# Performance work log

Hardware: AMD Instinct MI355X
Metric: run time of the kernel (lower is better)

Reference implementation:

```python
import jax, jax.numpy as jnp
import numpy as np

N = 10000      # atoms
E = 160000     # edges (avg degree 16)
H = 64         # hidden_channels
R = 64         # num_rbf
MAXZ = 100
RC = 4.5       # cutoff_upper (cutoff_lower = 0)
LN_EPS = 1e-5


def setup_inputs() -> dict:
    key = jax.random.key(0)
    ks = jax.random.split(key, 20)
    z = jax.random.randint(ks[0], (N,), 0, MAXZ, dtype=jnp.int32)
    edge_index = jax.random.randint(ks[1], (2, E), 0, N, dtype=jnp.int32)
    edge_weight = jax.random.uniform(ks[2], (E,), dtype=jnp.float32) * RC
    v = jax.random.normal(ks[3], (E, 3), dtype=jnp.float32)
    edge_vec_norm = v / jnp.linalg.norm(v, axis=-1, keepdims=True)
    edge_attr = jax.random.normal(ks[4], (E, R), dtype=jnp.float32)
    p = lambda k, shape: (jax.random.normal(k, shape, dtype=jnp.float32) * 0.1)
    return {
        'z': z, 'edge_index': edge_index, 'edge_weight': edge_weight,
        'edge_vec_norm': edge_vec_norm, 'edge_attr': edge_attr,
        'emb': p(ks[5], (MAXZ, H)),
        'emb2_w': p(ks[6], (H, 2 * H)), 'emb2_b': p(ks[7], (H,)),
        'dp1_w': p(ks[8], (H, R)), 'dp1_b': p(ks[9], (H,)),
        'dp2_w': p(ks[10], (H, R)), 'dp2_b': p(ks[11], (H,)),
        'dp3_w': p(ks[12], (H, R)), 'dp3_b': p(ks[13], (H,)),
        'ln_g': jnp.ones((H,), jnp.float32), 'ln_b': jnp.zeros((H,), jnp.float32),
        'w1': p(ks[14], (2 * H, H)), 'b1': jnp.zeros((2 * H,), jnp.float32),
        'w2': p(ks[15], (3 * H, 2 * H)), 'b2': jnp.zeros((3 * H,), jnp.float32),
        'm0': p(ks[16], (H, H)), 'm1': p(ks[17], (H, H)), 'm2': p(ks[18], (H, H)),
    }


def reference(z, edge_index, edge_weight, edge_vec_norm, edge_attr,
              emb, emb2_w, emb2_b, dp1_w, dp1_b, dp2_w, dp2_b, dp3_w, dp3_b,
              ln_g, ln_b, w1, b1, w2, b2, m0, m1, m2):
    n_atoms = z.shape[0]
    hc = emb.shape[1]
    src, dst = edge_index[0], edge_index[1]

    # atomic number message Z_ij: concat(Z_i, Z_j) -> Linear  [E,H]
    Zn = emb[z]
    Zij = jnp.concatenate([Zn[src], Zn[dst]], axis=-1) @ emb2_w.T + emb2_b

    # cosine cutoff (cutoff_lower == 0)
    C = 0.5 * (jnp.cos(edge_weight * jnp.pi / RC) + 1.0) * (edge_weight < RC)

    # RBF-gated per-edge channel weights, all [E,H]
    g1 = (edge_attr @ dp1_w.T + dp1_b) * C[:, None] * Zij
    g2 = (edge_attr @ dp2_w.T + dp2_b) * C[:, None] * Zij
    g3 = (edge_attr @ dp3_w.T + dp3_b) * C[:, None] * Zij

    eye = jnp.eye(3, dtype=Zij.dtype)
    vx, vy, vz = edge_vec_norm[:, 0], edge_vec_norm[:, 1], edge_vec_norm[:, 2]
    zero = jnp.zeros_like(vx)
    skew = jnp.stack([zero, -vz, vy, vz, zero, -vx, -vy, vx, zero], axis=-1).reshape(-1, 3, 3)
    outer = edge_vec_norm[:, :, None] * edge_vec_norm[:, None, :]  # [E,3,3], symmetric
    sym = outer - (jnp.trace(outer, axis1=-2, axis2=-1) / 3.0)[:, None, None] * eye

    # per-edge messages [E,H,3,3]
    Iij = g1[:, :, None, None] * eye
    Aij = g2[:, :, None, None] * skew[:, None, :, :]
    Sij = g3[:, :, None, None] * sym[:, None, :, :]

    # scatter-add to atoms
    I = jax.ops.segment_sum(Iij, src, num_segments=n_atoms)
    A = jax.ops.segment_sum(Aij, src, num_segments=n_atoms)
    S = jax.ops.segment_sum(Sij, src, num_segments=n_atoms)

    # tensor norm -> layernorm -> MLP1
    tn = ((I + A + S) ** 2).sum((-2, -1))  # [N,H]
    mu = tn.mean(-1, keepdims=True)
    var = ((tn - mu) ** 2).mean(-1, keepdims=True)
    norm = (tn - mu) / jnp.sqrt(var + LN_EPS) * ln_g + ln_b
    norm = jax.nn.silu(norm @ w1.T + b1)
    norm = jax.nn.silu(norm @ w2.T + b2)
    norm = norm.reshape(-1, hc, 3)
    n0 = norm[..., 0][:, :, None, None]

    # channel-mixing; NOTE: original code applies MLP2[1]/MLP2[2] to the
    # updated I and gates all three with norm[...,0] -- replicated faithfully.
    I = jnp.einsum('nhij,kh->nkij', I, m0) * n0
    A = jnp.einsum('nhij,kh->nkij', I, m1) * n0
    S = jnp.einsum('nhij,kh->nkij', I, m2) * n0
    return I + A + S
```

## Files before the change

kernel.cpp:

```cpp
#include <hip/hip_runtime.h>
#include <stdint.h>

#define NATOMS 10000
#define NEDGES 160000
#define RCUT   4.5f
#define CAP    64
#define ATGRID 2500
#define FGRID  1024

#define T_BYTES    ((size_t)NATOMS * 640 * 4)
#define CNT_OFF    (T_BYTES)
#define CNT_BYTES  ((size_t)NATOMS * 4)
#define REC_OFF    (CNT_OFF + CNT_BYTES)
#define REC_BYTES  ((size_t)NATOMS * CAP * 16)
#define EMB_OFF    (REC_OFF + REC_BYTES)
#define EMB_BYTES  ((size_t)100 * 64 * 2)
#define POS_OFF    (EMB_OFF + 0x4000)
#define POS_BYTES  ((size_t)NEDGES * 4)
#define ATTR2_OFF  (POS_OFF + 0xA0000)
#define ATTR2_BYTES ((size_t)NATOMS * CAP * 64 * 2)
#define WS_NEED    (ATTR2_OFF + ATTR2_BYTES)

typedef unsigned short u16;
typedef __bf16 bf16x8 __attribute__((ext_vector_type(8)));
typedef float  f32x4  __attribute__((ext_vector_type(4)));

#define MFMA16(a,b,c) __builtin_amdgcn_mfma_f32_16x16x32_bf16((a),(b),(c),0,0,0)
#define BFMAGIC 0x3F803F80u
#define MSK 0xffff0000u

__device__ __forceinline__ float uf(unsigned int u){ return __uint_as_float(u); }
__device__ __forceinline__ float b2f(u16 u){
  union { unsigned int i; float f; } v; v.i = ((unsigned int)u) << 16; return v.f;
}
__device__ __forceinline__ u16 f2b(float f){
  union { unsigned int i; float f; } v; v.f = f;
  unsigned int b = v.i + 0x7fffu + ((v.i >> 16) & 1u);
  return (u16)(b >> 16);
}
__device__ __forceinline__ float ldf(const void* p, int i, int bf){
  if (bf) return b2f(((const u16*)p)[i]);
  return ((const float*)p)[i];
}
__device__ __forceinline__ bf16x8 ld8bf(const void* p, int i, int bf){
  if (bf) return *(const bf16x8*)((const u16*)p + i);
  const float4* q = (const float4*)((const float*)p + i);
  float4 a = q[0], b = q[1];
  bf16x8 r;
  r[0]=(__bf16)a.x; r[1]=(__bf16)a.y; r[2]=(__bf16)a.z; r[3]=(__bf16)a.w;
  r[4]=(__bf16)b.x; r[5]=(__bf16)b.y; r[6]=(__bf16)b.z; r[7]=(__bf16)b.w;
  return r;
}
__device__ __forceinline__ uint4 ld8pk(const void* p, int i, int bf){
  if (bf) return *(const uint4*)((const u16*)p + i);
  const float4* q = (const float4*)((const float*)p + i);
  float4 a = q[0], b = q[1];
  uint4 r;
  r.x = (unsigned int)f2b(a.x) | ((unsigned int)f2b(a.y) << 16);
  r.y = (unsigned int)f2b(a.z) | ((unsigned int)f2b(a.w) << 16);
  r.z = (unsigned int)f2b(b.x) | ((unsigned int)f2b(b.y) << 16);
  r.w = (unsigned int)f2b(b.z) | ((unsigned int)f2b(b.w) << 16);
  return r;
}
__device__ __forceinline__ void ld8f(const void* p, int i, float* o, int bf){
  if (bf){
    uint4 v = *(const uint4*)((const u16*)p + i);
    o[0]=uf(v.x<<16); o[1]=uf(v.x&MSK); o[2]=uf(v.y<<16); o[3]=uf(v.y&MSK);
    o[4]=uf(v.z<<16); o[5]=uf(v.z&MSK); o[6]=uf(v.w<<16); o[7]=uf(v.w&MSK);
    return;
  }
  const float4* q = (const float4*)((const float*)p + i);
  float4 a = q[0], b = q[1];
  o[0]=a.x; o[1]=a.y; o[2]=a.z; o[3]=a.w; o[4]=b.x; o[5]=b.y; o[6]=b.z; o[7]=b.w;
}
__device__ __forceinline__ uint4 pk8(const float* f){
  uint4 r;
  r.x = (unsigned int)f2b(f[0]) | ((unsigned int)f2b(f[1]) << 16);
  r.y = (unsigned int)f2b(f[2]) | ((unsigned int)f2b(f[3]) << 16);
  r.z = (unsigned int)f2b(f[4]) | ((unsigned int)f2b(f[5]) << 16);
  r.w = (unsigned int)f2b(f[6]) | ((unsigned int)f2b(f[7]) << 16);
  return r;
}

__global__ __launch_bounds__(256) void scatter_kernel(const int* __restrict__ ei,
                                                      const int* __restrict__ z,
                                                      const void* __restrict__ ew,
                                                      const void* __restrict__ evn,
                                                      const void* __restrict__ emb,
                                                      u16* __restrict__ emb16,
                                                      int* __restrict__ cnt,
                                                      uint4* __restrict__ REC,
                                                      int* __restrict__ pos,
                                                      const unsigned int* __restrict__ lng){
  const int bf = (lng[0] == BFMAGIC);
  int e = blockIdx.x * 256 + threadIdx.x;
  if (e < 6400) emb16[e] = bf ? ((const u16*)emb)[e] : f2b(((const float*)emb)[e]);
  int s = ei[e], d = ei[NEDGES + e];
  int p = atomicAdd(&cnt[s], 1);
  const float w  = ldf(ew, e, bf);
  const float Cv = (w < RCUT) ? 0.5f*(__cosf(w * (3.14159265358979f / RCUT)) + 1.0f) : 0.0f;
  uint4 rec;
  rec.x = (unsigned int)e;
  rec.y = (unsigned int)z[d];
  rec.z = (unsigned int)f2b(ldf(evn, 3*e + 0, bf)) | ((unsigned int)f2b(ldf(evn, 3*e + 1, bf)) << 16);
  rec.w = (unsigned int)f2b(ldf(evn, 3*e + 2, bf)) | ((unsigned int)f2b(Cv) << 16);
  const int ok = (p < CAP);
  if (ok) REC[(size_t)s*CAP + p] = rec;
  if (pos) pos[e] = ok ? (s*CAP + p) : -1;
}

__global__ __launch_bounds__(256) void copy_kernel(const void* __restrict__ attr,
                                                   const int* __restrict__ pos,
                                                   u16* __restrict__ attr2,
                                                   const unsigned int* __restrict__ lng){
  const int bf  = (lng[0] == BFMAGIC);
  const int idx = blockIdx.x * 256 + threadIdx.x;
  const int e   = idx >> 3;
  const int c   = idx & 7;
  const int d   = pos[e];
  if (d >= 0)
    *(uint4*)(attr2 + (size_t)d*64 + c*8) = ld8pk(attr, e*64 + c*8, bf);
}

__global__ __launch_bounds__(256)
void atomT_stream(
    const int* __restrict__ z,
    const u16* __restrict__ emb16,
    const u16* __restrict__ attr2,
    const uint4* __restrict__ REC,
    const int* __restrict__ cnt,
    const void* __restrict__ e2w, const void* __restrict__ e2b,
    const void* __restrict__ d1w, const void* __restrict__ d1b,
    const void* __restrict__ d2w, const void* __restrict__ d2b,
    const void* __restrict__ d3w, const void* __restrict__ d3b,
    float* __restrict__ T,
    const unsigned int* __restrict__ lng)
{
  const int bf  = (lng[0] == BFMAGIC);
  const int tid = threadIdx.x;
  const int lane = tid & 63;
  const int wave = tid >> 6;
  const int hh   = lane & 15;
  const int quad = lane >> 4;
  const int h    = hh + 16*wave;

  const bf16x8 bw1a = ld8bf(d1w, h*64 + quad*8, bf);
  const bf16x8 bw1b = ld8bf(d1w, h*64 + 32 + quad*8, bf);
  const bf16x8 bw2a = ld8bf(d2w, h*64 + quad*8, bf);
  const bf16x8 bw2b = ld8bf(d2w, h*64 + 32 + quad*8, bf);
  const bf16x8 bw3a = ld8bf(d3w, h*64 + quad*8, bf);
  const bf16x8 bw3b = ld8bf(d3w, h*64 + 32 + quad*8, bf);
  const bf16x8 bea  = ld8bf(e2w, h*128 + quad*8, bf);
  const bf16x8 beb  = ld8bf(e2w, h*128 + 32 + quad*8, bf);
  const bf16x8 bec  = ld8bf(e2w, h*128 + 64 + quad*8, bf);
  const bf16x8 bed  = ld8bf(e2w, h*128 + 96 + quad*8, bf);

  const float be2 = ldf(e2b, h, bf);
  const float bd1 = ldf(d1b, h, bf);
  const float bd2 = ldf(d2b, h, bf);
  const float bd3 = ldf(d3b, h, bf);

  int n   = blockIdx.x;
  int cn  = cnt[n];
  int zsv = z[n];

  while (true) {
    const int e0   = n * CAP;
    const int nv   = min(cn, CAP);
    const int e1   = e0 + nv;
    const int e1m1 = (nv > 0) ? (e1 - 1) : e0;
    uint4 recA = REC[min(e0 + hh, e1m1)];

    bf16x8 zf0 = *(const bf16x8*)(emb16 + zsv*64 + quad*8);
    bf16x8 zf1 = *(const bf16x8*)(emb16 + zsv*64 + 32 + quad*8);

    const int nn   = n + ATGRID;
    const bool more = (nn < NATOMS);
    if (more){ cn = cnt[nn]; zsv = z[nn]; }

    float P[10];
#pragma unroll
    for (int c = 0; c < 10; c++) P[c] = 0.f;

    for (int base = e0; base < e1; base += 16){
      const size_t sA = (size_t)min(base + hh, e1 - 1) * 64;
      bf16x8 af0 = *(const bf16x8*)(attr2 + sA + quad*8);
      bf16x8 af1 = *(const bf16x8*)(attr2 + sA + 32 + quad*8);

      uint4 recN = REC[min(base + 16 + hh, e1 - 1)];

      bf16x8 zf2 = *(const bf16x8*)(emb16 + min(recA.y, 99u)*64 + quad*8);
      bf16x8 zf3 = *(const bf16x8*)(emb16 + min(recA.y, 99u)*64 + 32 + quad*8);

      f32x4 aZ = (f32x4){0.f,0.f,0.f,0.f};
      f32x4 a1 = (f32x4){0.f,0.f,0.f,0.f};
      f32x4 a2 = (f32x4){0.f,0.f,0.f,0.f};
      f32x4 a3 = (f32x4){0.f,0.f,0.f,0.f};

      a1 = MFMA16(af0, bw1a, a1);
      a1 = MFMA16(af1, bw1b, a1);
      a2 = MFMA16(af0, bw2a, a2);
      a2 = MFMA16(af1, bw2b, a2);
      a3 = MFMA16(af0, bw3a, a3);
      a3 = MFMA16(af1, bw3b, a3);
      aZ = MFMA16(zf0, bea, aZ);
      aZ = MFMA16(zf1, beb, aZ);
      aZ = MFMA16(zf2, bec, aZ);
      aZ = MFMA16(zf3, bed, aZ);

#pragma unroll
      for (int r = 0; r < 4; r++){
        const int ii = base + quad*4 + r;
        const bool ea = (ii < e1);
        const int srcl = quad*20 + r;
        const unsigned int rz = (unsigned int)__shfl((int)recA.z, srcl, 64);
        const unsigned int rw = (unsigned int)__shfl((int)recA.w, srcl, 64);
        const float Cv = ea ? b2f((u16)(rw >> 16)) : 0.f;
        const float vx = b2f((u16)(rz & 0xffffu));
        const float vy = b2f((u16)(rz >> 16));
        const float vz = b2f((u16)(rw & 0xffffu));
        const float xx = vx*vx - (1.f/3.f), yy = vy*vy - (1.f/3.f), zz = vz*vz - (1.f/3.f);
        const float xy = vx*vy, xz = vx*vz, yz = vy*vz;
        const float czv = Cv * (aZ[r] + be2);
        const float g1 = (a1[r] + bd1) * czv;
        const float g2 = (a2[r] + bd2) * czv;
        const float g3 = (a3[r] + bd3) * czv;
        P[0] += g1;
        P[1] += g2*vx; P[2] += g2*vy; P[3] += g2*vz;
        P[4] += g3*xx; P[5] += g3*yy; P[6] += g3*zz;
        P[7] += g3*xy; P[8] += g3*xz; P[9] += g3*yz;
      }
      recA = recN;
    }

#pragma unroll
    for (int c = 0; c < 10; c++){
      float v = P[c];
      v += __shfl_xor(v, 16, 64);
      v += __shfl_xor(v, 32, 64);
      P[c] = v;
    }

    if (quad == 0){
      float* Tn = T + (size_t)n * 640 + 16*wave + hh;
#pragma unroll
      for (int c = 0; c < 10; c++)
        Tn[c*64] = P[c];
    }

    if (!more) break;
    n = nn;
  }
}

__global__ __launch_bounds__(256)
void atomT_kernel(
    const int* __restrict__ z,
    const u16* __restrict__ emb16,
    const void* __restrict__ attr,
    const uint4* __restrict__ REC,
    const int* __restrict__ cnt,
    const void* __restrict__ e2w, const void* __restrict__ e2b,
    const void* __restrict__ d1w, const void* __restrict__ d1b,
    const void* __restrict__ d2w, const void* __restrict__ d2b,
    const void* __restrict__ d3w, const void* __restrict__ d3b,
    float* __restrict__ T,
    const unsigned int* __restrict__ lng)
{
  __shared__ __align__(16) u16 dpW[3][64][64];
  __shared__ __align__(16) u16 e2W[64][128];

  const int bf  = (lng[0] == BFMAGIC);
  const int tid = threadIdx.x;
  const void* dps[3] = {d1w, d2w, d3w};
  for (int idx = tid; idx < 1536; idx += 256){
    int w = idx >> 9, rem = idx & 511, r = rem >> 3, c8 = rem & 7;
    *(bf16x8*)&dpW[w][r][(c8 ^ (r & 7))*8] = ld8bf(dps[w], r*64 + c8*8, bf);
  }
  for (int idx = tid; idx < 1024; idx += 256){
    int r = idx >> 4, c8 = idx & 15;
    *(bf16x8*)&e2W[r][(c8 ^ (r & 7))*8] = ld8bf(e2w, r*128 + c8*8, bf);
  }
  __syncthreads();

  const int lane = tid & 63;
  const int wave = tid >> 6;
  const int hh   = lane & 15;
  const int quad = lane >> 4;
  const int half = wave & 1;
  const int ntb  = half * 2;
  const int wpair = wave >> 1;

  float be2[2], bd1[2], bd2[2], bd3[2];
#pragma unroll
  for (int j = 0; j < 2; j++){
    int h = hh + 16*(ntb + j);
    be2[j] = ldf(e2b, h, bf); bd1[j] = ldf(d1b, h, bf);
    bd2[j] = ldf(d2b, h, bf); bd3[j] = ldf(d3b, h, bf);
  }

  int pr  = blockIdx.x;
  int n   = pr * 2 + wpair;
  int cn  = cnt[n];
  int zsv = z[n];

  while (true) {
    const int e0   = n * CAP;
    const int nv   = min(cn, CAP);
    const int e1   = e0 + nv;
    const int e1m1 = (nv > 0) ? (e1 - 1) : e0;
    uint4 recA = REC[min(e0 + hh, e1m1)];

    bf16x8 zf0 = *(const bf16x8*)(emb16 + zsv*64 + quad*8);
    bf16x8 zf1 = *(const bf16x8*)(emb16 + zsv*64 + 32 + quad*8);

    const int prn  = pr + FGRID;
    const bool more = (prn < NATOMS/2);
    const int nn   = prn * 2 + wpair;
    if (more){ cn = cnt[nn]; zsv = z[nn]; }

    float P[10][2];
#pragma unroll
    for (int c = 0; c < 10; c++){ P[c][0] = 0.f; P[c][1] = 0.f; }

    for (int base = e0; base < e1; base += 16){
      uint4 recN = REC[min(base + 16 + hh, e1 - 1)];

      bf16x8 af0 = ld8bf(attr, (int)recA.x*64 + quad*8, bf);
      bf16x8 af1 = ld8bf(attr, (int)recA.x*64 + 32 + quad*8, bf);
      bf16x8 zf2 = *(const bf16x8*)(emb16 + recA.y*64 + quad*8);
      bf16x8 zf3 = *(const bf16x8*)(emb16 + recA.y*64 + 32 + quad*8);

      f32x4 aZ[2], a1[2], a2[2], a3[2];
#pragma unroll
      for (int j = 0; j < 2; j++){
        aZ[j] = (f32x4){0.f,0.f,0.f,0.f};
        a1[j] = (f32x4){0.f,0.f,0.f,0.f};
        a2[j] = (f32x4){0.f,0.f,0.f,0.f};
        a3[j] = (f32x4){0.f,0.f,0.f,0.f};
      }

#pragma unroll
      for (int j = 0; j < 2; j++){
        const int h  = hh + 16*(ntb + j);
        const int s0 = (quad       ^ (h & 7)) * 8;
        const int s1 = ((quad + 4) ^ (h & 7)) * 8;
        bf16x8 b;
        b = *(const bf16x8*)&dpW[0][h][s0];           a1[j] = MFMA16(af0, b, a1[j]);
        b = *(const bf16x8*)&dpW[0][h][s1];           a1[j] = MFMA16(af1, b, a1[j]);
        b = *(const bf16x8*)&dpW[1][h][s0];           a2[j] = MFMA16(af0, b, a2[j]);
        b = *(const bf16x8*)&dpW[1][h][s1];           a2[j] = MFMA16(af1, b, a2[j]);
        b = *(const bf16x8*)&dpW[2][h][s0];           a3[j] = MFMA16(af0, b, a3[j]);
        b = *(const bf16x8*)&dpW[2][h][s1];           a3[j] = MFMA16(af1, b, a3[j]);
        b = *(const bf16x8*)&e2W[h][s0];              aZ[j] = MFMA16(zf0, b, aZ[j]);
        b = *(const bf16x8*)&e2W[h][s1];              aZ[j] = MFMA16(zf1, b, aZ[j]);
        b = *(const bf16x8*)&e2W[h][((quad + 8)  ^ (h & 7)) * 8];  aZ[j] = MFMA16(zf2, b, aZ[j]);
        b = *(const bf16x8*)&e2W[h][((quad + 12) ^ (h & 7)) * 8];  aZ[j] = MFMA16(zf3, b, aZ[j]);
      }

#pragma unroll
      for (int r = 0; r < 4; r++){
        const int ii = base + quad*4 + r;
        const bool ea = (ii < e1);
        const int srcl = quad*20 + r;
        const unsigned int rz = (unsigned int)__shfl((int)recA.z, srcl, 64);
        const unsigned int rw = (unsigned int)__shfl((int)recA.w, srcl, 64);
        const float Cv = ea ? b2f((u16)(rw >> 16)) : 0.f;
        const float vx = b2f((u16)(rz & 0xffffu));
        const float vy = b2f((u16)(rz >> 16));
        const float vz = b2f((u16)(rw & 0xffffu));
        const float xx = vx*vx - (1.f/3.f), yy = vy*vy - (1.f/3.f), zz = vz*vz - (1.f/3.f);
        const float xy = vx*vy, xz = vx*vz, yz = vy*vz;
#pragma unroll
        for (int j = 0; j < 2; j++){
          const float czv = Cv * (aZ[j][r] + be2[j]);
          const float g1 = (a1[j][r] + bd1[j]) * czv;
          const float g2 = (a2[j][r] + bd2[j]) * czv;
          const float g3 = (a3[j][r] + bd3[j]) * czv;
          P[0][j] += g1;
          P[1][j] += g2*vx; P[2][j] += g2*vy; P[3][j] += g2*vz;
          P[4][j] += g3*xx; P[5][j] += g3*yy; P[6][j] += g3*zz;
          P[7][j] += g3*xy; P[8][j] += g3*xz; P[9][j] += g3*yz;
        }
      }
      recA = recN;
    }

#pragma unroll
    for (int c = 0; c < 10; c++)
#pragma unroll
      for (int j = 0; j < 2; j++){
        float v = P[c][j];
        v += __shfl_xor(v, 16, 64);
        v += __shfl_xor(v, 32, 64);
        P[c][j] = v;
      }

    if ((quad >> 1) == half){
      float* Tn = T + (size_t)n * 640;
#pragma unroll
      for (int c = 0; c < 10; c++)
        Tn[c*64 + lane] = P[c][quad & 1];
    }

    if (!more) break;
    pr = prn; n = nn;
  }
}

__global__ __launch_bounds__(256) void mlp_kernel(
    const float* __restrict__ T,
    const void* __restrict__ ln_g, const void* __restrict__ ln_b,
    const void* __restrict__ w1,  const void* __restrict__ b1,
    const void* __restrict__ w2,  const void* __restrict__ b2p,
    const void* __restrict__ m0,  const void* __restrict__ m1,
    const void* __restrict__ m2,  void* __restrict__ out,
    const unsigned int* __restrict__ lng)
{
  __shared__ __align__(16) u16 w1L[128][72];
  __shared__ __align__(16) u16 w2L[64][136];
  __shared__ __align__(16) u16 m0L[64][72];
  __shared__ __align__(16) u16 msL[64][72];
  __shared__ __align__(16) float xbuf[4][64];
  __shared__ __align__(16) float hbuf2[4][128];
  __shared__ __align__(16) float isoB[4][64];
  __shared__ __align__(16) float i1B[4][64];

  const int bf  = (lng[0] == BFMAGIC);
  const int tid = threadIdx.x;

  for (int idx = tid; idx < 1024; idx += 256){
    int r = idx >> 3, c8 = idx & 7;
    *(uint4*)&w1L[r][c8*8] = ld8pk(w1, r*64 + c8*8, bf);
  }
  for (int idx = tid; idx < 1024; idx += 256){
    int r = idx >> 4, c8 = idx & 15;
    *(uint4*)&w2L[r][c8*8] = ld8pk(w2, (3*r)*128 + c8*8, bf);
  }
  for (int idx = tid; idx < 512; idx += 256){
    int r = idx >> 3, c8 = idx & 7;
    *(uint4*)&m0L[r][c8*8] = ld8pk(m0, r*64 + c8*8, bf);
    float f[8], g[8];
    ld8f(m1, r*64 + c8*8, f, bf);
    ld8f(m2, r*64 + c8*8, g, bf);
#pragma unroll
    for (int q = 0; q < 8; q++) f[q] += g[q];
    *(uint4*)&msL[r][c8*8] = pk8(f);
  }
  __syncthreads();

  const int wave = tid >> 6;
  const int h    = tid & 63;
  const int wid  = blockIdx.x * 4 + wave;

  const float lngh = ldf(ln_g, h, bf), lnbh = ldf(ln_b, h, bf);
  const float b1a = ldf(b1, h, bf), b1b = ldf(b1, h + 64, bf);
  const float b2h = ldf(b2p, 3*h, bf);

  const uint4*  A4 = (const uint4*)&w1L[h][0];
  const uint4*  B4 = (const uint4*)&w1L[h + 64][0];
  const uint4*  W4 = (const uint4*)&w2L[h][0];
  const uint4*  M4 = (const uint4*)&m0L[h][0];
  const uint4*  S4 = (const uint4*)&msL[h][0];
  const float4* X4  = (const float4*)&xbuf[wave][0];
  const float4* H4  = (const float4*)&hbuf2[wave][0];
  const float4* I4  = (const float4*)&isoB[wave][0];
  const float4* J4  = (const float4*)&i1B[wave][0];

  const int NITER = (NATOMS + 2047) / 2048;
  for (int it = 0; it < NITER; it++){
    const int n   = wid + it * 2048;
    const bool act = (n < NATOMS);
    const int na  = act ? n : 0;

    const float* Tn = T + (size_t)na * 640;
    const float iso = Tn[h];
    const float wx = Tn[64+h], wy = Tn[128+h], wz = Tn[192+h];
    const float sxx = Tn[256+h], syy = Tn[320+h], szz = Tn[384+h];
    const float sxy = Tn[448+h], sxz = Tn[512+h], syz = Tn[576+h];
    const float tn = (iso+sxx)*(iso+sxx) + (iso+syy)*(iso+syy) + (iso+szz)*(iso+szz)
                   + 2.f*(sxy*sxy + sxz*sxz + syz*syz + wx*wx + wy*wy + wz*wz);
    isoB[wave][h] = iso;

    float s = tn;
#pragma unroll
    for (int off = 32; off; off >>= 1) s += __shfl_xor(s, off, 64);
    const float mu = s * (1.f/64.f);
    const float d0 = tn - mu;
    float v = d0 * d0;
#pragma unroll
    for (int off = 32; off; off >>= 1) v += __shfl_xor(v, off, 64);
    v *= (1.f/64.f);
    xbuf[wave][h] = d0 * rsqrtf(v + 1e-5f) * lngh + lnbh;
    __syncthreads();

    float acc0 = b1a, acc1 = b1b;
#pragma unroll
    for (int q = 0; q < 8; q++){
      const uint4 A = A4[q], B = B4[q];
      const float4 x0 = X4[2*q], x1 = X4[2*q + 1];
      acc0 += uf(A.x << 16)*x0.x + uf(A.x & MSK)*x0.y;
      acc0 += uf(A.y << 16)*x0.z + uf(A.y & MSK)*x0.w;
      acc0 += uf(A.z << 16)*x1.x + uf(A.z & MSK)*x1.y;
      acc0 += uf(A.w << 16)*x1.z + uf(A.w & MSK)*x1.w;
      acc1 += uf(B.x << 16)*x0.x + uf(B.x & MSK)*x0.y;
      acc1 += uf(B.y << 16)*x0.z + uf(B.y & MSK)*x0.w;
      acc1 += uf(B.z << 16)*x1.x + uf(B.z & MSK)*x1.y;
      acc1 += uf(B.w << 16)*x1.z + uf(B.w & MSK)*x1.w;
    }
    acc0 = acc0 / (1.f + __expf(-acc0));
    acc1 = acc1 / (1.f + __expf(-acc1));
    hbuf2[wave][h] = acc0; hbuf2[wave][h + 64] = acc1;
    __syncthreads();

    float acc2 = b2h, t1 = 0.f;
#pragma unroll
    for (int q = 0; q < 16; q++){
      const uint4 W = W4[q];
      const float4 y0 = H4[2*q], y1 = H4[2*q + 1];
      acc2 += uf(W.x << 16)*y0.x + uf(W.x & MSK)*y0.y;
      acc2 += uf(W.y << 16)*y0.z + uf(W.y & MSK)*y0.w;
      acc2 += uf(W.z << 16)*y1.x + uf(W.z & MSK)*y1.y;
      acc2 += uf(W.w << 16)*y1.z + uf(W.w & MSK)*y1.w;
    }
#pragma unroll
    for (int q = 0; q < 8; q++){
      const uint4 M = M4[q];
      const float4 x0 = I4[2*q], x1 = I4[2*q + 1];
      t1 += uf(M.x << 16)*x0.x + uf(M.x & MSK)*x0.y;
      t1 += uf(M.y << 16)*x0.z + uf(M.y & MSK)*x0.w;
      t1 += uf(M.z << 16)*x1.x + uf(M.z & MSK)*x1.y;
      t1 += uf(M.w << 16)*x1.z + uf(M.w & MSK)*x1.w;
    }
    const float n0 = acc2 / (1.f + __expf(-acc2));
    const float iso1 = t1 * n0;
    i1B[wave][h] = iso1;
    __syncthreads();

    float t23 = 0.f;
#pragma unroll
    for (int q = 0; q < 8; q++){
      const uint4 M = S4[q];
      const float4 x0 = J4[2*q], x1 = J4[2*q + 1];
      t23 += uf(M.x << 16)*x0.x + uf(M.x & MSK)*x0.y;
      t23 += uf(M.y << 16)*x0.z + uf(M.y & MSK)*x0.w;
      t23 += uf(M.z << 16)*x1.x + uf(M.z & MSK)*x1.y;
      t23 += uf(M.w << 16)*x1.z + uf(M.w & MSK)*x1.w;
    }
    const float dval = iso1 + t23 * n0;

    if (act){
      if (bf){
        u16* o = (u16*)out + (size_t)n * 576 + h * 9;
        const u16 db = f2b(dval);
        o[0] = db; o[1] = 0; o[2] = 0;
        o[3] = 0;  o[4] = db; o[5] = 0;
        o[6] = 0;  o[7] = 0;  o[8] = db;
      } else {
        float* o = (float*)out + (size_t)n * 576 + h * 9;
        o[0] = dval; o[1] = 0.f; o[2] = 0.f;
        o[3] = 0.f;  o[4] = dval; o[5] = 0.f;
        o[6] = 0.f;  o[7] = 0.f;  o[8] = dval;
      }
    }
    __syncthreads();
  }
}

extern "C" void kernel_launch(void* const* d_in, const int* in_sizes, int n_in,
                              void* d_out, int out_size, void* d_ws, size_t ws_size,
                              hipStream_t stream) {
  const int* z    = (const int*)d_in[0];
  const int* ei   = (const int*)d_in[1];
  const void* ew   = d_in[2];
  const void* evn  = d_in[3];
  const void* attr = d_in[4];
  const void* emb  = d_in[5];
  const void* e2w  = d_in[6];
  const void* e2b  = d_in[7];
  const void* d1w  = d_in[8];
  const void* d1b  = d_in[9];
  const void* d2w  = d_in[10];
  const void* d2b  = d_in[11];
  const void* d3w  = d_in[12];
  const void* d3b  = d_in[13];
  const void* ln_g = d_in[14];
  const void* ln_b = d_in[15];
  const void* w1   = d_in[16];
  const void* b1   = d_in[17];
  const void* w2   = d_in[18];
  const void* b2p  = d_in[19];
  const void* m0   = d_in[20];
  const void* m1   = d_in[21];
  const void* m2   = d_in[22];
  const unsigned int* lng = (const unsigned int*)ln_g;

  char* ws = (char*)d_ws;
  float*   T     = (float*)ws;
  int*     cnt   = (int*)(ws + CNT_OFF);
  uint4*   REC   = (uint4*)(ws + REC_OFF);
  u16*     emb16 = (u16*)(ws + EMB_OFF);
  const int big  = (ws_size >= WS_NEED);
  int*     pos   = big ? (int*)(ws + POS_OFF) : nullptr;
  u16*     attr2 = big ? (u16*)(ws + ATTR2_OFF) : nullptr;

  hipMemsetAsync(cnt, 0, CNT_BYTES, stream);
  scatter_kernel<<<NEDGES/256, 256, 0, stream>>>(ei, z, ew, evn, emb, emb16, cnt, REC,
                                                 pos, lng);
  if (big){
    copy_kernel<<<NEDGES*8/256, 256, 0, stream>>>(attr, pos, attr2, lng);
    atomT_stream<<<ATGRID, 256, 0, stream>>>(z, emb16, attr2, REC, cnt, e2w, e2b,
                                             d1w, d1b, d2w, d2b, d3w, d3b, T, lng);
  } else {
    atomT_kernel<<<FGRID, 256, 0, stream>>>(z, emb16, attr, REC, cnt, e2w, e2b,
                                            d1w, d1b, d2w, d2b, d3w, d3b, T, lng);
  }
  mlp_kernel<<<512, 256, 0, stream>>>(T, ln_g, ln_b, w1, b1, w2, b2p,
                                      m0, m1, m2, d_out, lng);
}
```

Before: 242.5 us.

## Fuse edge-attribute copy into scatter kernel and shrink atomT_stream grid

The separate copy_kernel and its global pos array are removed. Each scatter block now keeps its slot indices in shared memory and copies the 64-wide edge_attr rows into the atom-ordered bf16 buffer itself. This saves one kernel launch plus the pos write and read round trip. The atomT_stream grid also drops from 2500 to 1024 blocks, which presumably relies on a grid-stride loop over atoms and changes load balance and occupancy.

```diff
diff --git a/kernel.cpp b/kernel.cpp
--- a/kernel.cpp
+++ b/kernel.cpp
@@ -5,7 +5,7 @@
 #define NEDGES 160000
 #define RCUT   4.5f
 #define CAP    64
-#define ATGRID 2500
+#define ATGRID 1024
 #define FGRID  1024
 
 #define T_BYTES    ((size_t)NATOMS * 640 * 4)
@@ -15,9 +15,7 @@
 #define REC_BYTES  ((size_t)NATOMS * CAP * 16)
 #define EMB_OFF    (REC_OFF + REC_BYTES)
 #define EMB_BYTES  ((size_t)100 * 64 * 2)
-#define POS_OFF    (EMB_OFF + 0x4000)
-#define POS_BYTES  ((size_t)NEDGES * 4)
-#define ATTR2_OFF  (POS_OFF + 0xA0000)
+#define ATTR2_OFF  (EMB_OFF + 0x4000)
 #define ATTR2_BYTES ((size_t)NATOMS * CAP * 64 * 2)
 #define WS_NEED    (ATTR2_OFF + ATTR2_BYTES)
 
@@ -90,10 +88,13 @@
                                                       u16* __restrict__ emb16,
                                                       int* __restrict__ cnt,
                                                       uint4* __restrict__ REC,
-                                                      int* __restrict__ pos,
+                                                      const void* __restrict__ attr,
+                                                      u16* __restrict__ attr2,
                                                       const unsigned int* __restrict__ lng){
-  const int bf = (lng[0] == BFMAGIC);
-  int e = blockIdx.x * 256 + threadIdx.x;
+  __shared__ int posL[256];
+  const int bf  = (lng[0] == BFMAGIC);
+  const int tid = threadIdx.x;
+  const int e   = blockIdx.x * 256 + tid;
   if (e < 6400) emb16[e] = bf ? ((const u16*)emb)[e] : f2b(((const float*)emb)[e]);
   int s = ei[e], d = ei[NEDGES + e];
   int p = atomicAdd(&cnt[s], 1);
@@ -106,20 +107,21 @@
   rec.w = (unsigned int)f2b(ldf(evn, 3*e + 2, bf)) | ((unsigned int)f2b(Cv) << 16);
   const int ok = (p < CAP);
   if (ok) REC[(size_t)s*CAP + p] = rec;
-  if (pos) pos[e] = ok ? (s*CAP + p) : -1;
-}
-
-__global__ __launch_bounds__(256) void copy_kernel(const void* __restrict__ attr,
-                                                   const int* __restrict__ pos,
-                                                   u16* __restrict__ attr2,
-                                                   const unsigned int* __restrict__ lng){
-  const int bf  = (lng[0] == BFMAGIC);
-  const int idx = blockIdx.x * 256 + threadIdx.x;
-  const int e   = idx >> 3;
-  const int c   = idx & 7;
-  const int d   = pos[e];
-  if (d >= 0)
-    *(uint4*)(attr2 + (size_t)d*64 + c*8) = ld8pk(attr, e*64 + c*8, bf);
+
+  if (!attr2) return;
+  posL[tid] = ok ? (s*CAP + p) : -1;
+  __syncthreads();
+
+  const int e0 = blockIdx.x * 256;
+#pragma unroll
+  for (int it = 0; it < 8; it++){
+    const int idx = it * 256 + tid;
+    const int eb  = idx >> 3;
+    const int c   = idx & 7;
+    const int dp  = posL[eb];
+    if (dp >= 0)
+      *(uint4*)(attr2 + (size_t)dp*64 + c*8) = ld8pk(attr, (e0 + eb)*64 + c*8, bf);
+  }
 }
 
 __global__ __launch_bounds__(256)
@@ -601,14 +603,12 @@
   uint4*   REC   = (uint4*)(ws + REC_OFF);
   u16*     emb16 = (u16*)(ws + EMB_OFF);
   const int big  = (ws_size >= WS_NEED);
-  int*     pos   = big ? (int*)(ws + POS_OFF) : nullptr;
   u16*     attr2 = big ? (u16*)(ws + ATTR2_OFF) : nullptr;
 
   hipMemsetAsync(cnt, 0, CNT_BYTES, stream);
   scatter_kernel<<<NEDGES/256, 256, 0, stream>>>(ei, z, ew, evn, emb, emb16, cnt, REC,
-                                                 pos, lng);
+                                                 attr, attr2, lng);
   if (big){
-    copy_kernel<<<NEDGES*8/256, 256, 0, stream>>>(attr, pos, attr2, lng);
     atomT_stream<<<ATGRID, 256, 0, stream>>>(z, emb16, attr2, REC, cnt, e2w, e2b,
                                              d1w, d1b, d2w, d2b, d3w, d3b, T, lng);
   } else {
```

Result: faster. 234.8 us (-3.2%).
